# Kernel tuning notes

Hardware: AMD Instinct MI355X
Metric: run time of the kernel (lower is better)

## Reference

```python
import jax, jax.numpy as jnp
import numpy as np

N_NODES = 50000
N_EDGES = 800000
DIM = 128
HEADS = 4
NEG_SLOPE = 0.2
LN_EPS = 1e-5


def setup_inputs() -> dict:
    key = jax.random.key(0)
    ks = jax.random.split(key, 8)
    x = jax.random.normal(ks[0], (N_NODES, DIM), dtype=jnp.float32)
    edge_index = jax.random.randint(ks[1], (2, N_EDGES), 0, N_NODES, dtype=jnp.int32)
    W = jax.random.normal(ks[2], (DIM, DIM), dtype=jnp.float32) * (1.0 / np.sqrt(DIM))
    b = jnp.zeros((DIM,), dtype=jnp.float32)
    C = DIM // HEADS
    att_src = jax.random.normal(ks[3], (HEADS, C), dtype=jnp.float32) * 0.1
    att_dst = jax.random.normal(ks[4], (HEADS, C), dtype=jnp.float32) * 0.1
    ln_gamma = jnp.ones((DIM,), dtype=jnp.float32)
    ln_beta = jnp.zeros((DIM,), dtype=jnp.float32)
    prelu_w = jnp.full((1,), 0.25, dtype=jnp.float32)
    return {"x": x, "edge_index": edge_index, "W": W, "b": b,
            "att_src": att_src, "att_dst": att_dst,
            "ln_gamma": ln_gamma, "ln_beta": ln_beta, "prelu_w": prelu_w}


def reference(x, edge_index, W, b, att_src, att_dst, ln_gamma, ln_beta, prelu_w):
    N, D = x.shape
    H = HEADS
    C = D // H
    # shared linear transform (PyG GATConv lin_src == lin_dst for homogeneous input)
    xw = (x @ W).reshape(N, H, C)                      # [N,H,C]
    a_src = jnp.einsum('nhc,hc->nh', xw, att_src)      # [N,H]
    a_dst = jnp.einsum('nhc,hc->nh', xw, att_dst)      # [N,H]
    # add self loops (PyG default add_self_loops=True)
    loop = jnp.arange(N, dtype=edge_index.dtype)
    src = jnp.concatenate([edge_index[0], loop])       # [E+N]
    dst = jnp.concatenate([edge_index[1], loop])       # [E+N]
    # per-edge attention logits + segment softmax over destination
    alpha = jax.nn.leaky_relu(a_src[src] + a_dst[dst], NEG_SLOPE)   # [E+N,H]
    amax = jax.ops.segment_max(alpha, dst, num_segments=N)          # [N,H]
    alpha = jnp.exp(alpha - amax[dst])
    denom = jax.ops.segment_sum(alpha, dst, num_segments=N)         # [N,H]
    alpha = alpha / denom[dst]
    # weighted aggregation of source features
    msg = xw[src] * alpha[:, :, None]                               # [E+N,H,C]
    out = jax.ops.segment_sum(msg, dst, num_segments=N).reshape(N, D) + b
    # residual + LayerNorm + PReLU
    h = x + out
    mu = jnp.mean(h, axis=-1, keepdims=True)
    var = jnp.mean(jnp.square(h - mu), axis=-1, keepdims=True)
    h = (h - mu) * jax.lax.rsqrt(var + LN_EPS) * ln_gamma + ln_beta
    return jnp.where(h > 0, h, prelu_w[0] * h)
```

## Files before the change

### kernel.cpp

```cpp
#include <hip/hip_runtime.h>

#define NNODES 50000
#define NEDGES 800000
#define NEDGE4 200000
#define DIMF 128
#define NHEADS 4
#define NEG_SLOPE 0.2f
#define LN_EPS 1e-5f
#define SLOTS 64
#define NPERX 6250
#define NLB 782
#define SCB 2048

typedef int   v4i   __attribute__((ext_vector_type(4)));
typedef float v2f   __attribute__((ext_vector_type(2)));
typedef short bf16x8 __attribute__((ext_vector_type(8)));
typedef float f32x4  __attribute__((ext_vector_type(4)));
typedef unsigned short u16x8 __attribute__((ext_vector_type(8)));

__device__ __forceinline__ unsigned short f2bf(float f) {
    unsigned int u = __float_as_uint(f);
    u = (u + 0x7fffu + ((u >> 16) & 1u)) >> 16;
    return (unsigned short)u;
}
__device__ __forceinline__ float bf2f(unsigned short u) {
    return __uint_as_float(((unsigned int)u) << 16);
}

__global__ __launch_bounds__(256) void k_prep(const float* __restrict__ W,
                                              unsigned short* __restrict__ WtG,
                                              int* __restrict__ cursor)
{
    const int idx = blockIdx.x * 256 + threadIdx.x;
    if (idx < DIMF * DIMF) {
        const int k = idx >> 7, col = idx & 127;
        WtG[col * 136 + k] = f2bf(W[idx]);
    }
    if (idx < NNODES) cursor[idx] = 0;
}

__global__ __launch_bounds__(256) void k_linear(
    const float* __restrict__ x, const unsigned short* __restrict__ WtG,
    const float* __restrict__ att_src, const float* __restrict__ att_dst,
    unsigned short* __restrict__ xwb,
    float* __restrict__ asrc, float* __restrict__ adst)
{
    __shared__ unsigned short WtL[128 * 136];
    __shared__ float sAttS[128], sAttD[128];
    const int tid  = threadIdx.x;
    const int base = blockIdx.x * 64;

    if (tid < 128) sAttS[tid] = att_src[tid];
    else           sAttD[tid - 128] = att_dst[tid - 128];
    {
        const uint4* g = (const uint4*)WtG;
        uint4* l = (uint4*)WtL;
        for (int i = tid; i < 2176; i += 256) l[i] = g[i];
    }
    __syncthreads();

    const int wv_   = tid >> 6;
    const int lane  = tid & 63;
    const int row16 = lane & 15;
    const int kg    = lane >> 4;
    const int grow_a = base + wv_ * 16 + row16;
    const int arow   = (grow_a < NNODES) ? grow_a : 0;

    f32x4 acc[8];
    #pragma unroll
    for (int ct = 0; ct < 8; ++ct) acc[ct] = (f32x4){0.f, 0.f, 0.f, 0.f};

    #pragma unroll
    for (int ks = 0; ks < 4; ++ks) {
        const float4* xr = (const float4*)(x + (size_t)arow * DIMF + ks * 32 + kg * 8);
        const float4 xa = xr[0], xb = xr[1];
        bf16x8 af;
        af[0] = (short)f2bf(xa.x); af[1] = (short)f2bf(xa.y);
        af[2] = (short)f2bf(xa.z); af[3] = (short)f2bf(xa.w);
        af[4] = (short)f2bf(xb.x); af[5] = (short)f2bf(xb.y);
        af[6] = (short)f2bf(xb.z); af[7] = (short)f2bf(xb.w);
        #pragma unroll
        for (int ct = 0; ct < 8; ++ct) {
            const bf16x8 bfr = *(const bf16x8*)&WtL[(ct * 16 + row16) * 136 + ks * 32 + kg * 8];
            acc[ct] = __builtin_amdgcn_mfma_f32_16x16x32_bf16(af, bfr, acc[ct], 0, 0, 0);
        }
    }

    __syncthreads();
    unsigned short* OutL = WtL;
    #pragma unroll
    for (int ct = 0; ct < 8; ++ct) {
        #pragma unroll
        for (int r = 0; r < 4; ++r)
            OutL[(wv_ * 16 + kg * 4 + r) * 136 + ct * 16 + row16] = f2bf(acc[ct][r]);
    }
    __syncthreads();

    const int row = tid >> 2, seg = tid & 3;
    const int grow = base + row;
    if (grow < NNODES) {
        const u16x8* srcv = (const u16x8*)&OutL[row * 136 + seg * 32];
        u16x8* dstv = (u16x8*)(xwb + (size_t)grow * DIMF + seg * 32);
        float ps = 0.f, pd = 0.f;
        #pragma unroll
        for (int q = 0; q < 4; ++q) {
            const u16x8 v = srcv[q];
            dstv[q] = v;
            #pragma unroll
            for (int j = 0; j < 8; ++j) {
                const float f = bf2f(v[j]);
                const int c = seg * 32 + q * 8 + j;
                ps += f * sAttS[c];
                pd += f * sAttD[c];
            }
        }
        asrc[grow * NHEADS + seg] = ps;
        adst[grow * NHEADS + seg] = pd;
    }
}

__global__ __launch_bounds__(256) void k_scatter(
    const int* __restrict__ esrc, const int* __restrict__ edst,
    int* __restrict__ cursor, unsigned short* __restrict__ perm)
{
    const int lo = (blockIdx.x & 7) * NPERX, hi = lo + NPERX;
    const int stride = (SCB >> 3) * 256;
    const v4i* es4 = (const v4i*)esrc;
    const v4i* ed4 = (const v4i*)edst;
    for (int e = (blockIdx.x >> 3) * 256 + threadIdx.x; e < NEDGE4; e += stride) {
        v4i d4 = __builtin_nontemporal_load(ed4 + e);
        v4i s4 = __builtin_nontemporal_load(es4 + e);
        #pragma unroll
        for (int c = 0; c < 4; ++c) {
            const int dd = d4[c], ss = s4[c];
            if (dd >= lo && dd < hi) {
                int p = atomicAdd(&cursor[dd], 1);
                if (p < SLOTS) perm[(size_t)dd * SLOTS + p] = (unsigned short)ss;
            }
        }
    }
}

__global__ __launch_bounds__(256) void k_weights(
    const float4* __restrict__ asrc4, const float4* __restrict__ adst4,
    const int* __restrict__ cursor, const unsigned short* __restrict__ perm,
    ushort4* __restrict__ wperm)
{
    const int wid  = (blockIdx.x * 256 + threadIdx.x) >> 6;
    const int lane = threadIdx.x & 63;
    if (wid >= NNODES) return;

    int cnt = cursor[wid];
    if (cnt > SLOTS) cnt = SLOTS;
    const int cnt2 = (cnt + 15) & ~15;
    const float4 dv = adst4[wid];

    ushort4 wu = make_ushort4(0, 0, 0, 0);
    if (lane < cnt) {
        const int s = (int)perm[(size_t)wid * SLOTS + lane];
        const float4 ae = asrc4[s];
        float l0 = ae.x + dv.x, l1 = ae.y + dv.y;
        float l2 = ae.z + dv.z, l3 = ae.w + dv.w;
        l0 = (l0 > 0.f) ? l0 : NEG_SLOPE * l0;
        l1 = (l1 > 0.f) ? l1 : NEG_SLOPE * l1;
        l2 = (l2 > 0.f) ? l2 : NEG_SLOPE * l2;
        l3 = (l3 > 0.f) ? l3 : NEG_SLOPE * l3;
        wu.x = f2bf(__expf(l0)); wu.y = f2bf(__expf(l1));
        wu.z = f2bf(__expf(l2)); wu.w = f2bf(__expf(l3));
    }
    if (lane < cnt2) wperm[(size_t)wid * SLOTS + lane] = wu;
}

__global__ __launch_bounds__(256) void k_gat(
    const float* __restrict__ x, const float* __restrict__ bias,
    const float* __restrict__ asrc, const float* __restrict__ adst,
    const unsigned int* __restrict__ xwb,
    const int* __restrict__ cursor, const unsigned short* __restrict__ perm,
    const unsigned short* __restrict__ wperm_u16,
    const float* __restrict__ ln_g, const float* __restrict__ ln_b,
    const float* __restrict__ prelu_w, float* __restrict__ out)
{
    const int wid  = (blockIdx.x * 256 + threadIdx.x) >> 6;
    const int lane = threadIdx.x & 63;
    if (wid >= NNODES) return;
    const int myh = lane >> 4;
    const int hb  = lane & 3;

    const float adh_b = adst[wid * NHEADS + hb];
    float lgS = asrc[wid * NHEADS + hb] + adh_b;
    lgS = (lgS > 0.f) ? lgS : NEG_SLOPE * lgS;
    const float wself_b = __expf(lgS);

    int cnt = cursor[wid];
    if (cnt > SLOTS) cnt = SLOTS;
    const int sidx = (lane < cnt) ? (int)perm[(size_t)wid * SLOTS + lane] : 0;

    const float wself = __shfl(wself_b, myh);
    const unsigned int vself = xwb[(size_t)wid * 64 + lane];
    float acc0 = wself * __uint_as_float(vself << 16);
    float acc1 = wself * __uint_as_float(vself & 0xffff0000u);
    float dsum = 0.f;

    const int jmax = (cnt + 15) >> 4;
    for (int j = 0; j < jmax; ++j) {
        const unsigned short wu = wperm_u16[(size_t)wid * 256 + j * 64 + lane];
        const float wv = __uint_as_float(((unsigned)wu) << 16);
        dsum += wv;

        #pragma unroll
        for (int b = 0; b < 2; ++b) {
            const int ebase = j * 16 + b * 8;
            int s_[8]; float w_[8]; unsigned v_[8];
            #pragma unroll
            for (int e = 0; e < 8; ++e) {
                s_[e] = __shfl(sidx, ebase + e);
                w_[e] = __shfl(wv, ((b * 8 + e) << 2) | myh);
            }
            #pragma unroll
            for (int e = 0; e < 8; ++e)
                v_[e] = xwb[(size_t)s_[e] * 64 + lane];
            #pragma unroll
            for (int e = 0; e < 8; ++e) {
                acc0 += w_[e] * __uint_as_float(v_[e] << 16);
                acc1 += w_[e] * __uint_as_float(v_[e] & 0xffff0000u);
            }
        }
    }

    #pragma unroll
    for (int o = 4; o < 64; o <<= 1) dsum += __shfl_xor(dsum, o);
    const float wsum = __shfl(dsum + wself_b, myh);

    const float inv = 1.0f / wsum;
    const int c = lane * 2;
    const float2 xr = ((const float2*)x)[(size_t)wid * 64 + lane];
    float h0 = xr.x + acc0 * inv + bias[c];
    float h1 = xr.y + acc1 * inv + bias[c + 1];

    float s1 = h0 + h1, s2 = h0 * h0 + h1 * h1;
    #pragma unroll
    for (int o = 1; o < 64; o <<= 1) {
        s1 += __shfl_xor(s1, o);
        s2 += __shfl_xor(s2, o);
    }
    const float mu  = s1 * (1.f / 128.f);
    const float var = s2 * (1.f / 128.f) - mu * mu;
    const float r   = rsqrtf(var + LN_EPS);

    float g0 = (h0 - mu) * r * ln_g[c]     + ln_b[c];
    float g1 = (h1 - mu) * r * ln_g[c + 1] + ln_b[c + 1];
    const float pw = prelu_w[0];
    g0 = (g0 > 0.f) ? g0 : pw * g0;
    g1 = (g1 > 0.f) ? g1 : pw * g1;

    v2f gv; gv.x = g0; gv.y = g1;
    __builtin_nontemporal_store(gv, (v2f*)out + (size_t)wid * 64 + lane);
}

extern "C" void kernel_launch(void* const* d_in, const int* in_sizes, int n_in,
                              void* d_out, int out_size, void* d_ws, size_t ws_size,
                              hipStream_t stream)
{
    const float* x    = (const float*)d_in[0];
    const int*   eidx = (const int*)  d_in[1];
    const float* W    = (const float*)d_in[2];
    const float* bias = (const float*)d_in[3];
    const float* attS = (const float*)d_in[4];
    const float* attD = (const float*)d_in[5];
    const float* lng  = (const float*)d_in[6];
    const float* lnb  = (const float*)d_in[7];
    const float* pre  = (const float*)d_in[8];

    const int* esrc = eidx;
    const int* edst = eidx + NEDGES;

    unsigned short* xwb = (unsigned short*)d_ws;
    float* asrc    = (float*)(xwb + (size_t)NNODES * DIMF);
    float* adst    = asrc + (size_t)NNODES * NHEADS;
    int*   cursor  = (int*)(adst + (size_t)NNODES * NHEADS);
    unsigned short* perm = (unsigned short*)(cursor + NNODES);
    ushort4* wperm = (ushort4*)(perm + (size_t)NNODES * SLOTS);
    unsigned short* WtG = (unsigned short*)(wperm + (size_t)NNODES * SLOTS);

    k_prep<<<dim3(196), dim3(256), 0, stream>>>(W, WtG, cursor);

    k_linear<<<dim3(NLB), dim3(256), 0, stream>>>(
        x, WtG, attS, attD, xwb, asrc, adst);

    k_scatter<<<dim3(SCB), dim3(256), 0, stream>>>(esrc, edst, cursor, perm);

    k_weights<<<dim3((NNODES * 64 + 255) / 256), dim3(256), 0, stream>>>(
        (const float4*)asrc, (const float4*)adst, cursor, perm, wperm);

    k_gat<<<dim3((NNODES * 64 + 255) / 256), dim3(256), 0, stream>>>(
        x, bias, asrc, adst, (const unsigned int*)xwb, cursor, perm,
        (const unsigned short*)wperm, lng, lnb, pre, (float*)d_out);
}
```

Measured before the change: 116.5 us.

## Merge linear and edge-scatter kernels into one launch with split LDS staging

Combines the independent linear-transform kernel and the edge scatter kernel into a single launch whose block index selects the role, so the compute-bound GEMM and the atomic-bound scatter can run on the GPU at the same time. The W tile in shared memory is halved and loaded in two passes, with the x fragments preloaded into registers, which lowers LDS use per block and allows higher occupancy. Loads of x and stores of xwb are now nontemporal. The cost is extra barriers and two rounds of W loads per block, and the scatter blocks are scheduled before the GEMM blocks.

```diff
diff --git a/kernel.cpp b/kernel.cpp
--- a/kernel.cpp
+++ b/kernel.cpp
@@ -14,6 +14,7 @@
 
 typedef int   v4i   __attribute__((ext_vector_type(4)));
 typedef float v2f   __attribute__((ext_vector_type(2)));
+typedef float v4f   __attribute__((ext_vector_type(4)));
 typedef short bf16x8 __attribute__((ext_vector_type(8)));
 typedef float f32x4  __attribute__((ext_vector_type(4)));
 typedef unsigned short u16x8 __attribute__((ext_vector_type(8)));
@@ -39,25 +40,42 @@
     if (idx < NNODES) cursor[idx] = 0;
 }
 
-__global__ __launch_bounds__(256) void k_linear(
+__global__ __launch_bounds__(256) void k_main(
     const float* __restrict__ x, const unsigned short* __restrict__ WtG,
     const float* __restrict__ att_src, const float* __restrict__ att_dst,
     unsigned short* __restrict__ xwb,
-    float* __restrict__ asrc, float* __restrict__ adst)
-{
-    __shared__ unsigned short WtL[128 * 136];
+    float* __restrict__ asrc, float* __restrict__ adst,
+    const int* __restrict__ esrc, const int* __restrict__ edst,
+    int* __restrict__ cursor, unsigned short* __restrict__ perm)
+{
+    __shared__ unsigned short WtL[64 * 136];
     __shared__ float sAttS[128], sAttD[128];
-    const int tid  = threadIdx.x;
-    const int base = blockIdx.x * 64;
+    const int tid = threadIdx.x;
+
+    if (blockIdx.x < SCB) {
+        const int lo = (blockIdx.x & 7) * NPERX, hi = lo + NPERX;
+        const v4i* es4 = (const v4i*)esrc;
+        const v4i* ed4 = (const v4i*)edst;
+        const int stride = (SCB >> 3) * 256;
+        for (int e = (blockIdx.x >> 3) * 256 + tid; e < NEDGE4; e += stride) {
+            v4i d4 = __builtin_nontemporal_load(ed4 + e);
+            v4i s4 = __builtin_nontemporal_load(es4 + e);
+            #pragma unroll
+            for (int c = 0; c < 4; ++c) {
+                const int dd = d4[c], ss = s4[c];
+                if (dd >= lo && dd < hi) {
+                    int p = atomicAdd(&cursor[dd], 1);
+                    if (p < SLOTS) perm[(size_t)dd * SLOTS + p] = (unsigned short)ss;
+                }
+            }
+        }
+        return;
+    }
+
+    const int base = (blockIdx.x - SCB) * 64;
 
     if (tid < 128) sAttS[tid] = att_src[tid];
     else           sAttD[tid - 128] = att_dst[tid - 128];
-    {
-        const uint4* g = (const uint4*)WtG;
-        uint4* l = (uint4*)WtL;
-        for (int i = tid; i < 2176; i += 256) l[i] = g[i];
-    }
-    __syncthreads();
 
     const int wv_   = tid >> 6;
     const int lane  = tid & 63;
@@ -66,23 +84,35 @@
     const int grow_a = base + wv_ * 16 + row16;
     const int arow   = (grow_a < NNODES) ? grow_a : 0;
 
+    bf16x8 af[4];
+    #pragma unroll
+    for (int ks = 0; ks < 4; ++ks) {
+        const v4f* xr = (const v4f*)(x + (size_t)arow * DIMF + ks * 32 + kg * 8);
+        const v4f xa = __builtin_nontemporal_load(xr);
+        const v4f xb = __builtin_nontemporal_load(xr + 1);
+        af[ks][0] = (short)f2bf(xa.x); af[ks][1] = (short)f2bf(xa.y);
+        af[ks][2] = (short)f2bf(xa.z); af[ks][3] = (short)f2bf(xa.w);
+        af[ks][4] = (short)f2bf(xb.x); af[ks][5] = (short)f2bf(xb.y);
+        af[ks][6] = (short)f2bf(xb.z); af[ks][7] = (short)f2bf(xb.w);
+    }
+
     f32x4 acc[8];
     #pragma unroll
     for (int ct = 0; ct < 8; ++ct) acc[ct] = (f32x4){0.f, 0.f, 0.f, 0.f};
 
-    #pragma unroll
-    for (int ks = 0; ks < 4; ++ks) {
-        const float4* xr = (const float4*)(x + (size_t)arow * DIMF + ks * 32 + kg * 8);
-        const float4 xa = xr[0], xb = xr[1];
-        bf16x8 af;
-        af[0] = (short)f2bf(xa.x); af[1] = (short)f2bf(xa.y);
-        af[2] = (short)f2bf(xa.z); af[3] = (short)f2bf(xa.w);
-        af[4] = (short)f2bf(xb.x); af[5] = (short)f2bf(xb.y);
-        af[6] = (short)f2bf(xb.z); af[7] = (short)f2bf(xb.w);
+    const uint4* g = (const uint4*)WtG;
+    for (int hf = 0; hf < 2; ++hf) {
+        __syncthreads();
+        for (int i = tid; i < 1088; i += 256)
+            ((uint4*)WtL)[i] = g[hf * 1088 + i];
+        __syncthreads();
         #pragma unroll
-        for (int ct = 0; ct < 8; ++ct) {
-            const bf16x8 bfr = *(const bf16x8*)&WtL[(ct * 16 + row16) * 136 + ks * 32 + kg * 8];
-            acc[ct] = __builtin_amdgcn_mfma_f32_16x16x32_bf16(af, bfr, acc[ct], 0, 0, 0);
+        for (int ks = 0; ks < 4; ++ks) {
+            #pragma unroll
+            for (int ct = 0; ct < 4; ++ct) {
+                const bf16x8 bfr = *(const bf16x8*)&WtL[(ct * 16 + row16) * 136 + ks * 32 + kg * 8];
+                acc[hf * 4 + ct] = __builtin_amdgcn_mfma_f32_16x16x32_bf16(af[ks], bfr, acc[hf * 4 + ct], 0, 0, 0);
+            }
         }
     }
 
@@ -105,7 +135,7 @@
         #pragma unroll
         for (int q = 0; q < 4; ++q) {
             const u16x8 v = srcv[q];
-            dstv[q] = v;
+            __builtin_nontemporal_store(v, dstv + q);
             #pragma unroll
             for (int j = 0; j < 8; ++j) {
                 const float f = bf2f(v[j]);
@@ -116,28 +146,6 @@
         }
         asrc[grow * NHEADS + seg] = ps;
         adst[grow * NHEADS + seg] = pd;
-    }
-}
-
-__global__ __launch_bounds__(256) void k_scatter(
-    const int* __restrict__ esrc, const int* __restrict__ edst,
-    int* __restrict__ cursor, unsigned short* __restrict__ perm)
-{
-    const int lo = (blockIdx.x & 7) * NPERX, hi = lo + NPERX;
-    const int stride = (SCB >> 3) * 256;
-    const v4i* es4 = (const v4i*)esrc;
-    const v4i* ed4 = (const v4i*)edst;
-    for (int e = (blockIdx.x >> 3) * 256 + threadIdx.x; e < NEDGE4; e += stride) {
-        v4i d4 = __builtin_nontemporal_load(ed4 + e);
-        v4i s4 = __builtin_nontemporal_load(es4 + e);
-        #pragma unroll
-        for (int c = 0; c < 4; ++c) {
-            const int dd = d4[c], ss = s4[c];
-            if (dd >= lo && dd < hi) {
-                int p = atomicAdd(&cursor[dd], 1);
-                if (p < SLOTS) perm[(size_t)dd * SLOTS + p] = (unsigned short)ss;
-            }
-        }
     }
 }
 
@@ -284,10 +292,8 @@
 
     k_prep<<<dim3(196), dim3(256), 0, stream>>>(W, WtG, cursor);
 
-    k_linear<<<dim3(NLB), dim3(256), 0, stream>>>(
-        x, WtG, attS, attD, xwb, asrc, adst);
-
-    k_scatter<<<dim3(SCB), dim3(256), 0, stream>>>(esrc, edst, cursor, perm);
+    k_main<<<dim3(SCB + NLB), dim3(256), 0, stream>>>(
+        x, WtG, attS, attD, xwb, asrc, adst, esrc, edst, cursor, perm);
 
     k_weights<<<dim3((NNODES * 64 + 255) / 256), dim3(256), 0, stream>>>(
         (const float4*)asrc, (const float4*)adst, cursor, perm, wperm);
```

Result: faster. 110.4 us (-5.3%).
